# Performance work log

Measured on AMD Instinct MI355X. Metric: run time of the kernel, lower is better.

Reference implementation:

```python
import jax, jax.numpy as jnp
import numpy as np
from jax import lax

N, D, M, H = 8192, 32, 8, 128
ATOL = 1e-5
RTOL = 1e-5
MAX_STEPS = 10   # bounded adaptive dopri5 iterations (accept/reject with masking)
DT0 = 0.25


def setup_inputs() -> dict:
    key = jax.random.key(0)
    ks = jax.random.split(key, 6)
    p = lambda k, shape, s: jax.random.normal(k, shape, jnp.float32) * s
    return {
        "z": jax.random.normal(ks[0], (N, D), jnp.float32),
        "G_w": p(ks[1], (M, D), 0.3),
        "W1": p(ks[2], (H, D), (1.0 / D) ** 0.5),
        "b1": jnp.zeros((H,), jnp.float32),
        "W2": p(ks[3], (H, H), (1.0 / H) ** 0.5),
        "b2": jnp.zeros((H,), jnp.float32),
        "W3": p(ks[4], (D, H), (1.0 / H) ** 0.5),
        "b3": jnp.zeros((D,), jnp.float32),
        "T": jnp.ones((1,), jnp.float32),
    }


def qpnf_forward(z, G_w, W1, b1, W2, b2, W3, b3, T):
    d = z.shape[1]

    def mlp(x):  # dF network: d -> 128 -> 128 -> d
        h = jax.nn.relu(x @ W1.T + b1)
        h = jax.nn.relu(h @ W2.T + b2)
        return h @ W3.T + b3

    # G is linear (no bias) so jacrev(G)(x) == G_w for every sample; the batched
    # dG @ dG^T solves collapse to one shared (m,m) solve / (d,d) projector.
    A = G_w @ G_w.T                       # (m, m)
    AinvG = jnp.linalg.solve(A, G_w)      # (m, d) = A^{-1} W
    P = G_w.T @ AinvG                     # (d, d) null-space projector W^T A^{-1} W
    IP = jnp.eye(d, dtype=z.dtype) - P
    trP = jnp.trace(P)

    jac_mlp = jax.vmap(jax.jacrev(lambda xi: mlp(xi[None, :])[0]))  # (N,d,d)

    def f(y):  # augmented state y = [x | logp], dlogp/dt = -div(dx/dx)
        x = y[:, :d]
        dF = mlp(x)                        # (N, d)
        g = x @ G_w.T                      # (N, m)
        dz = -(dF @ IP) - g @ AinvG        # -(eta_J) - (eta_C)
        JdF = jac_mlp(x)                   # (N, d, d)
        # J_f = -(I-P) JdF - P  ->  dlogp = -trace(J_f)
        dlogp = jnp.einsum('jk,nkj->n', IP, JdF) + trP
        return jnp.concatenate([dz, dlogp[:, None]], axis=1)

    def rk_step(y, dt):  # Dormand-Prince 5(4)
        k1 = f(y)
        k2 = f(y + dt * (0.2 * k1))
        k3 = f(y + dt * (3/40 * k1 + 9/40 * k2))
        k4 = f(y + dt * (44/45 * k1 - 56/15 * k2 + 32/9 * k3))
        k5 = f(y + dt * (19372/6561 * k1 - 25360/2187 * k2 + 64448/6561 * k3 - 212/729 * k4))
        k6 = f(y + dt * (9017/3168 * k1 - 355/33 * k2 + 46732/5247 * k3 + 49/176 * k4 - 5103/18656 * k5))
        y1 = y + dt * (35/384 * k1 + 500/1113 * k3 + 125/192 * k4 - 2187/6784 * k5 + 11/84 * k6)
        k7 = f(y1)
        err = dt * ((35/384 - 5179/57600) * k1 + (500/1113 - 7571/16695) * k3
                    + (125/192 - 393/640) * k4 + (-2187/6784 + 92097/339200) * k5
                    + (11/84 - 187/2100) * k6 - (1/40) * k7)
        return y1, err

    t1 = 2.0 * T[0]  # eval path: integration_times[-1] *= 2
    y0 = jnp.concatenate([z, jnp.zeros((z.shape[0], 1), z.dtype)], axis=1)

    def body(carry, _):
        t, dt, y = carry
        done = t >= t1 - 1e-9
        dtc = jnp.where(done, jnp.asarray(1e-3, z.dtype), jnp.minimum(dt, t1 - t))
        y1, ev = rk_step(y, dtc)
        tol = ATOL + RTOL * jnp.maximum(jnp.abs(y), jnp.abs(y1))
        errn = jnp.sqrt(jnp.mean((ev / tol) ** 2))
        accept = jnp.logical_and(~done, errn <= 1.0)
        y_new = jnp.where(accept, y1, y)
        t_new = jnp.where(accept, t + dtc, t)
        factor = jnp.clip(0.9 * errn ** (-0.2), 0.2, 10.0)
        dt_new = jnp.where(done, dt, jnp.clip(dtc * factor, 1e-6, t1))
        dt_new = lax.stop_gradient(dt_new)
        return (t_new, dt_new, y_new), None

    init = (jnp.asarray(0.0, z.dtype), jnp.asarray(DT0, z.dtype), y0)
    (_, _, yT), _ = lax.scan(body, init, None, length=MAX_STEPS)
    return yT[:, :d]


def reference(z, G_w, W1, b1, W2, b2, W3, b3, T):
    return qpnf_forward(z, G_w, W1, b1, W2, b2, W3, b3, T)
```

## Files before the change

kernel.cpp:

```cpp
#include <hip/hip_runtime.h>
#include <hip/hip_cooperative_groups.h>
#include <math.h>

namespace cg = cooperative_groups;
typedef float4 f4;
typedef float2 f2;
typedef float v2f __attribute__((ext_vector_type(2)));

#define NT 512
#define RB 32

#define WS_WR    0
#define WS_PART  32768
#define WS_TOTAL 35328

#define L_W1T   0
#define L_C3T   4096
#define L_PT    8320
#define L_XW    9472
#define L_H1W   10496
#define L_H2W   14592
#define L_KZ    18688
#define L_KL    26752
#define L_YZ    26976
#define L_Y1Z   28128
#define L_YL    29280
#define L_Y1L   29312
#define L_B1    29344
#define L_B2    29472
#define L_C0    29600
#define L_GS    29632
#define L_AAUG  29888
#define L_AINVG 30016
#define L_MISC  30272
#define LDS_FLOATS 30276
#define L_RED   L_H1W
#define L_P     L_H2W
#define L_IP    (L_H2W + 1024)
#define L_IPW3  L_KZ

__device__ const float ACO[5][5] = {
  { 0.2f, 0.f, 0.f, 0.f, 0.f },
  { (float)(3.0/40.0), (float)(9.0/40.0), 0.f, 0.f, 0.f },
  { (float)(44.0/45.0), (float)(-56.0/15.0), (float)(32.0/9.0), 0.f, 0.f },
  { (float)(19372.0/6561.0), (float)(-25360.0/2187.0), (float)(64448.0/6561.0), (float)(-212.0/729.0), 0.f },
  { (float)(9017.0/3168.0), (float)(-355.0/33.0), (float)(46732.0/5247.0), (float)(49.0/176.0), (float)(-5103.0/18656.0) }
};

#define B1C ((float)(35.0/384.0))
#define B3C ((float)(500.0/1113.0))
#define B4C ((float)(125.0/192.0))
#define B5C ((float)(-2187.0/6784.0))
#define B6C ((float)(11.0/84.0))

#define E1C ((float)(35.0/384.0 - 5179.0/57600.0))
#define E3C ((float)(500.0/1113.0 - 7571.0/16695.0))
#define E4C ((float)(125.0/192.0 - 393.0/640.0))
#define E5C ((float)(-2187.0/6784.0 + 92097.0/339200.0))
#define E6C ((float)(11.0/84.0 - 187.0/2100.0))
#define E7C ((float)(-1.0/40.0))

__device__ __forceinline__ f4 ld4(const float* p){ return *(const f4*)p; }
__device__ __forceinline__ void st4(float* p, f4 v){ *(f4*)p = v; }

__device__ __forceinline__ void pk_lo(v2f& d, v2f s, v2f b){
  asm("v_pk_fma_f32 %0, %1, %2, %0 op_sel:[0,0,0] op_sel_hi:[0,1,1]"
      : "+v"(d) : "v"(s), "v"(b));
}
__device__ __forceinline__ void pk_hi(v2f& d, v2f s, v2f b){
  asm("v_pk_fma_f32 %0, %1, %2, %0 op_sel:[1,0,0] op_sel_hi:[1,1,1]"
      : "+v"(d) : "v"(s), "v"(b));
}
__device__ __forceinline__ v2f vlo(f4 v){ v2f r; r.x = v.x; r.y = v.y; return r; }
__device__ __forceinline__ v2f vhi(f4 v){ v2f r; r.x = v.z; r.y = v.w; return r; }

__device__ __forceinline__ void assemble_x(float* lds, int tid, float dtc,
                                           const float* co, int np)
{
  const int w = tid >> 6, lane = tid & 63;
  const int r = lane >> 4;
  const int c = (lane << 1) & 31;
  const int o = (4 * w + r) * 36 + c;
  f2 y = *(const f2*)&lds[L_YZ + o];
  float sx = 0.f, sy = 0.f;
  for (int p = 0; p < np; p++){
    f2 kv = *(const f2*)&lds[L_KZ + p * 1152 + o];
    sx += co[p] * kv.x; sy += co[p] * kv.y;
  }
  float* XWp = &lds[L_XW + w * 128];
  XWp[(c + 0) * 4 + r] = y.x + dtc * sx;
  XWp[(c + 1) * 4 + r] = y.y + dtc * sy;
}

__device__ void eval_f(float* lds, const float* __restrict__ ws, int tid,
                       float trP, int kout)
{
  const int w = tid >> 6, lane = tid & 63;
  const int cg = lane & 31, kh = lane >> 5;
  float* XWp = &lds[L_XW  + w * 128];
  float* H1p = &lds[L_H1W + w * 512];
  float* H2p = &lds[L_H2W + w * 512];

  const f4* WR4 = (const f4*)&ws[WS_WR];
  const int kb = kh * 64;
  const int grot = (w & 1) << 3;
  f4 wbA[4], rbA[4], wbB[4], rbB[4];
  {
    const int kA = kb + grot * 4;
    const int kB = kb + (grot + 1) * 4;
#pragma unroll
    for (int u = 0; u < 4; u++){
      wbA[u] = WR4[(kA + u) * 64 + cg];
      rbA[u] = WR4[(kA + u) * 64 + 32 + cg];
      wbB[u] = WR4[(kB + u) * 64 + cg];
      rbB[u] = WR4[(kB + u) * 64 + 32 + cg];
    }
  }

  v2f a12[4][2];
#pragma unroll
  for (int i = 0; i < 4; i++)
#pragma unroll
    for (int jp = 0; jp < 2; jp++){ a12[i][jp].x = 0.f; a12[i][jp].y = 0.f; }
#pragma unroll 4
  for (int t = 0; t < 16; t++){
    const int k = kh * 16 + t;
    f4 xv = ld4(&XWp[k * 4]);
    f4 wv = ld4(&lds[L_W1T + k * 128 + 4 * cg]);
    v2f x0 = vlo(xv), x1 = vhi(xv);
    v2f wA = vlo(wv), wB = vhi(wv);
    pk_lo(a12[0][0], wA, x0); pk_lo(a12[0][1], wA, x1);
    pk_hi(a12[1][0], wA, x0); pk_hi(a12[1][1], wA, x1);
    pk_lo(a12[2][0], wB, x0); pk_lo(a12[2][1], wB, x1);
    pk_hi(a12[3][0], wB, x0); pk_hi(a12[3][1], wB, x1);
  }
  float a1s[4][4];
#pragma unroll
  for (int i = 0; i < 4; i++){
    a1s[i][0] = a12[i][0].x; a1s[i][1] = a12[i][0].y;
    a1s[i][2] = a12[i][1].x; a1s[i][3] = a12[i][1].y;
  }
#pragma unroll
  for (int i = 0; i < 4; i++)
#pragma unroll
    for (int j = 0; j < 4; j++) a1s[i][j] += __shfl_xor(a1s[i][j], 32);
  if (kh == 0){
    f4 b1v = ld4(&lds[L_B1 + 4 * cg]);
    const float* b1p = (const float*)&b1v;
#pragma unroll
    for (int i = 0; i < 4; i++){
      f4 hv; float* hp = (float*)&hv;
#pragma unroll
      for (int j = 0; j < 4; j++){
        float pre = a1s[i][j] + b1p[i];
        hp[j] = fmaxf(pre, 0.f);
      }
      st4(&H1p[(4 * cg + i) * 4], hv);
    }
  }

  v2f ah2[4][2], at2[4][2];
#pragma unroll
  for (int i = 0; i < 4; i++)
#pragma unroll
    for (int jp = 0; jp < 2; jp++){
      ah2[i][jp].x = 0.f; ah2[i][jp].y = 0.f;
      at2[i][jp].x = 0.f; at2[i][jp].y = 0.f;
    }
#pragma unroll 1
  for (int gp = 0; gp < 8; gp++){
    {
      f4 wc[4], rc[4];
#pragma unroll
      for (int u = 0; u < 4; u++){ wc[u] = wbA[u]; rc[u] = rbA[u]; }
      if (gp < 7){
        const int kn = kb + (((2 * gp + 2) + grot) & 15) * 4;
#pragma unroll
        for (int u = 0; u < 4; u++){
          wbA[u] = WR4[(kn + u) * 64 + cg];
          rbA[u] = WR4[(kn + u) * 64 + 32 + cg];
        }
      }
      const int kc = kb + ((2 * gp + grot) & 15) * 4;
#pragma unroll
      for (int u = 0; u < 4; u++){
        f4 av = ld4(&H1p[(kc + u) * 4]);
        v2f a0 = vlo(av), a1 = vhi(av);
        v2f m0, m1;
        m0.x = (a0.x > 0.f) ? 1.f : 0.f; m0.y = (a0.y > 0.f) ? 1.f : 0.f;
        m1.x = (a1.x > 0.f) ? 1.f : 0.f; m1.y = (a1.y > 0.f) ? 1.f : 0.f;
        v2f wA = vlo(wc[u]), wB = vhi(wc[u]);
        v2f rA = vlo(rc[u]), rB = vhi(rc[u]);
        pk_lo(ah2[0][0], wA, a0); pk_lo(ah2[0][1], wA, a1);
        pk_hi(ah2[1][0], wA, a0); pk_hi(ah2[1][1], wA, a1);
        pk_lo(ah2[2][0], wB, a0); pk_lo(ah2[2][1], wB, a1);
        pk_hi(ah2[3][0], wB, a0); pk_hi(ah2[3][1], wB, a1);
        pk_lo(at2[0][0], rA, m0); pk_lo(at2[0][1], rA, m1);
        pk_hi(at2[1][0], rA, m0); pk_hi(at2[1][1], rA, m1);
        pk_lo(at2[2][0], rB, m0); pk_lo(at2[2][1], rB, m1);
        pk_hi(at2[3][0], rB, m0); pk_hi(at2[3][1], rB, m1);
      }
    }
    {
      f4 wc[4], rc[4];
#pragma unroll
      for (int u = 0; u < 4; u++){ wc[u] = wbB[u]; rc[u] = rbB[u]; }
      if (gp < 7){
        const int kn = kb + (((2 * gp + 3) + grot) & 15) * 4;
#pragma unroll
        for (int u = 0; u < 4; u++){
          wbB[u] = WR4[(kn + u) * 64 + cg];
          rbB[u] = WR4[(kn + u) * 64 + 32 + cg];
        }
      }
      const int kc = kb + (((2 * gp + 1) + grot) & 15) * 4;
#pragma unroll
      for (int u = 0; u < 4; u++){
        f4 av = ld4(&H1p[(kc + u) * 4]);
        v2f a0 = vlo(av), a1 = vhi(av);
        v2f m0, m1;
        m0.x = (a0.x > 0.f) ? 1.f : 0.f; m0.y = (a0.y > 0.f) ? 1.f : 0.f;
        m1.x = (a1.x > 0.f) ? 1.f : 0.f; m1.y = (a1.y > 0.f) ? 1.f : 0.f;
        v2f wA = vlo(wc[u]), wB = vhi(wc[u]);
        v2f rA = vlo(rc[u]), rB = vhi(rc[u]);
        pk_lo(ah2[0][0], wA, a0); pk_lo(ah2[0][1], wA, a1);
        pk_hi(ah2[1][0], wA, a0); pk_hi(ah2[1][1], wA, a1);
        pk_lo(ah2[2][0], wB, a0); pk_lo(ah2[2][1], wB, a1);
        pk_hi(ah2[3][0], wB, a0); pk_hi(ah2[3][1], wB, a1);
        pk_lo(at2[0][0], rA, m0); pk_lo(at2[0][1], rA, m1);
        pk_hi(at2[1][0], rA, m0); pk_hi(at2[1][1], rA, m1);
        pk_lo(at2[2][0], rB, m0); pk_lo(at2[2][1], rB, m1);
        pk_hi(at2[3][0], rB, m0); pk_hi(at2[3][1], rB, m1);
      }
    }
  }
  float ah[4][4], at[4][4];
#pragma unroll
  for (int i = 0; i < 4; i++){
    ah[i][0] = ah2[i][0].x; ah[i][1] = ah2[i][0].y;
    ah[i][2] = ah2[i][1].x; ah[i][3] = ah2[i][1].y;
    at[i][0] = at2[i][0].x; at[i][1] = at2[i][0].y;
    at[i][2] = at2[i][1].x; at[i][3] = at2[i][1].y;
  }
#pragma unroll
  for (int i = 0; i < 4; i++)
#pragma unroll
    for (int j = 0; j < 4; j++){
      ah[i][j] += __shfl_xor(ah[i][j], 32);
      at[i][j] += __shfl_xor(at[i][j], 32);
    }

  f4 b2v = ld4(&lds[L_B2 + 4 * cg]);
  const float* b2p = (const float*)&b2v;
  float h2v[4][4]; float dl[4] = {0.f, 0.f, 0.f, 0.f};
#pragma unroll
  for (int i = 0; i < 4; i++)
#pragma unroll
    for (int j = 0; j < 4; j++){
      float pre = ah[i][j] + b2p[i];
      float hv = fmaxf(pre, 0.f);
      h2v[i][j] = hv;
      if (pre > 0.f) dl[j] += at[i][j];
    }
#pragma unroll
  for (int mk = 1; mk < 32; mk <<= 1){
#pragma unroll
    for (int j = 0; j < 4; j++) dl[j] += __shfl_xor(dl[j], mk, 64);
  }
  if (kh == 0){
#pragma unroll
    for (int i = 0; i < 4; i++){
      f4 hv; float* hp = (float*)&hv;
#pragma unroll
      for (int j = 0; j < 4; j++) hp[j] = h2v[i][j];
      st4(&H2p[(4 * cg + i) * 4], hv);
    }
    if (cg == 0){
#pragma unroll
      for (int j = 0; j < 4; j++)
        lds[L_KL + kout * 32 + 4 * w + j] = dl[j] + trP;
    }
  }

  v2f a3e[2], a3o[2];
  a3e[0].x=0.f;a3e[0].y=0.f;a3e[1].x=0.f;a3e[1].y=0.f;
  a3o[0].x=0.f;a3o[0].y=0.f;a3o[1].x=0.f;a3o[1].y=0.f;
  const int bb = kh * 64;
#pragma unroll 4
  for (int t = 0; t < 16; t++){
    f4 cv = ld4(&lds[L_C3T + cg * 132 + bb + 4 * t]);
    v2f cA = vlo(cv), cB = vhi(cv);
    { f4 av = ld4(&H2p[(bb + 4 * t + 0) * 4]);
      pk_lo(a3e[0], cA, vlo(av)); pk_lo(a3e[1], cA, vhi(av)); }
    { f4 av = ld4(&H2p[(bb + 4 * t + 1) * 4]);
      pk_hi(a3o[0], cA, vlo(av)); pk_hi(a3o[1], cA, vhi(av)); }
    { f4 av = ld4(&H2p[(bb + 4 * t + 2) * 4]);
      pk_lo(a3e[0], cB, vlo(av)); pk_lo(a3e[1], cB, vhi(av)); }
    { f4 av = ld4(&H2p[(bb + 4 * t + 3) * 4]);
      pk_hi(a3o[0], cB, vlo(av)); pk_hi(a3o[1], cB, vhi(av)); }
  }
  const int qq = kh * 16;
#pragma unroll
  for (int t = 0; t < 4; t++){
    f4 pv = ld4(&lds[L_PT + cg * 36 + qq + 4 * t]);
    v2f pA = vlo(pv), pB = vhi(pv);
    { f4 av = ld4(&XWp[(qq + 4 * t + 0) * 4]);
      pk_lo(a3e[0], pA, vlo(av)); pk_lo(a3e[1], pA, vhi(av)); }
    { f4 av = ld4(&XWp[(qq + 4 * t + 1) * 4]);
      pk_hi(a3o[0], pA, vlo(av)); pk_hi(a3o[1], pA, vhi(av)); }
    { f4 av = ld4(&XWp[(qq + 4 * t + 2) * 4]);
      pk_lo(a3e[0], pB, vlo(av)); pk_lo(a3e[1], pB, vhi(av)); }
    { f4 av = ld4(&XWp[(qq + 4 * t + 3) * 4]);
      pk_hi(a3o[0], pB, vlo(av)); pk_hi(a3o[1], pB, vhi(av)); }
  }
  float a3[4];
  a3[0] = a3e[0].x + a3o[0].x; a3[1] = a3e[0].y + a3o[0].y;
  a3[2] = a3e[1].x + a3o[1].x; a3[3] = a3e[1].y + a3o[1].y;
#pragma unroll
  for (int j = 0; j < 4; j++) a3[j] += __shfl_xor(a3[j], 32);
  if (kh == 0){
    float c0v = lds[L_C0 + cg];
#pragma unroll
    for (int j = 0; j < 4; j++)
      lds[L_KZ + kout * 1152 + (4 * w + j) * 36 + cg] = -(a3[j] + c0v);
  }
}

__global__ void __launch_bounds__(NT, 2)
qpnf_kernel(const float* __restrict__ z, const float* __restrict__ Gw,
            const float* __restrict__ W1g, const float* __restrict__ b1g,
            const float* __restrict__ W2g, const float* __restrict__ b2g,
            const float* __restrict__ W3g, const float* __restrict__ b3g,
            const float* __restrict__ Tg, float* __restrict__ out,
            float* __restrict__ ws)
{
  __shared__ float lds[LDS_FLOATS];
  const int tid = threadIdx.x;
  const int bid = blockIdx.x;
  const int r0 = bid * RB;
  cg::grid_group grid = cg::this_grid();

  for (int i = 0; i < 8; i++){
    int idx = tid + i * NT;
    int h = idx >> 5, j = idx & 31;
    lds[L_W1T + j * 128 + h] = W1g[idx];
  }
  if (tid < 128){ lds[L_B1 + tid] = b1g[tid]; lds[L_B2 + tid] = b2g[tid]; }
  if (tid < 256) lds[L_GS + tid] = Gw[tid];
  __syncthreads();

  if (tid < 64){
    int i = tid >> 3, j = tid & 7;
    float s = 0.f;
    for (int k = 0; k < 32; k++) s += lds[L_GS + i * 32 + k] * lds[L_GS + j * 32 + k];
    lds[L_AAUG + i * 16 + j] = s;
    lds[L_AAUG + i * 16 + 8 + j] = (i == j) ? 1.f : 0.f;
  }
  __syncthreads();
  if (tid == 0){
    float* A = &lds[L_AAUG];
    for (int c = 0; c < 8; c++){
      int p = c; float mx = fabsf(A[c * 16 + c]);
      for (int r = c + 1; r < 8; r++){
        float v = fabsf(A[r * 16 + c]);
        if (v > mx){ mx = v; p = r; }
      }
      if (p != c)
        for (int q = 0; q < 16; q++){ float t = A[c*16+q]; A[c*16+q] = A[p*16+q]; A[p*16+q] = t; }
      float pv = 1.0f / A[c * 16 + c];
      for (int q = 0; q < 16; q++) A[c * 16 + q] *= pv;
      for (int r = 0; r < 8; r++) if (r != c){
        float fct = A[r * 16 + c];
        for (int q = 0; q < 16; q++) A[r * 16 + q] -= fct * A[c * 16 + q];
      }
    }
  }
  __syncthreads();
  if (tid < 256){
    int m = tid >> 5, d = tid & 31;
    float s = 0.f;
    for (int q = 0; q < 8; q++) s += lds[L_AAUG + m * 16 + 8 + q] * lds[L_GS + q * 32 + d];
    lds[L_AINVG + m * 32 + d] = s;
  }
  __syncthreads();
  for (int i4 = 0; i4 < 2; i4++){
    int idx = tid + i4 * NT;
    int i = idx >> 5, j = idx & 31;
    float s = 0.f;
    for (int m = 0; m < 8; m++) s += lds[L_GS + m * 32 + i] * lds[L_AINVG + m * 32 + j];
    lds[L_P + i * 32 + j] = s;
  }
  __syncthreads();
  float* IPl = &lds[L_IP];
  for (int i4 = 0; i4 < 2; i4++){
    int idx = tid + i4 * NT;
    int i = idx >> 5, j = idx & 31;
    IPl[i * 32 + j] = ((i == j) ? 1.f : 0.f) - lds[L_P + i * 32 + j];
  }
  if (tid == 0){
    float s = 0.f;
    for (int i = 0; i < 32; i++) s += lds[L_P + i * 32 + i];
    lds[L_MISC] = s;
  }
  __syncthreads();
  for (int i4 = 0; i4 < 8; i4++){
    int idx = tid + i4 * NT;
    int b = idx & 127, c = idx >> 7;
    float s = 0.f;
    for (int i = 0; i < 32; i++) s += W3g[i * 128 + b] * IPl[i * 32 + c];
    lds[L_C3T + c * 132 + b] = s;
  }
  for (int i4 = 0; i4 < 2; i4++){
    int idx = tid + i4 * NT;
    int c = idx >> 5, q = idx & 31;
    lds[L_PT + c * 36 + q] = lds[L_P + q * 32 + c];
  }
  if (tid < 32){
    float s = 0.f;
    for (int i = 0; i < 32; i++) s += b3g[i] * IPl[i * 32 + tid];
    lds[L_C0 + tid] = s;
  }
  for (int i4 = 0; i4 < 8; i4++){
    int idx = tid + i4 * NT;
    int j = idx >> 7, b = idx & 127;
    float s = 0.f;
    for (int k = 0; k < 32; k++) s += IPl[j * 32 + k] * W3g[k * 128 + b];
    lds[L_IPW3 + j * 128 + b] = s;
  }
  __syncthreads();
  if (bid < 128 && tid < 128){
    int a = bid;
    float s = 0.f;
    for (int j = 0; j < 32; j++) s += W1g[a * 32 + j] * lds[L_IPW3 + j * 128 + tid];
    ws[WS_WR + a * 256 + 128 + tid] = s * W2g[tid * 128 + a];
  }
  if (bid >= 128 && tid < 128){
    int a = bid - 128;
    ws[WS_WR + a * 256 + tid] = W2g[tid * 128 + a];
  }
  if (tid < 256){
    const int r = tid >> 3, jj = (tid & 7) * 4;
    st4(&lds[L_YZ + r * 36 + jj], ld4(&z[(r0 + r) * 32 + jj]));
  }
  if (tid < RB) lds[L_YL + tid] = 0.f;

  const float trP = lds[L_MISC];
  const float t1 = 2.0f * Tg[0];

  grid.sync();

  float t_cur = 0.f, dt_cur = 0.25f;
  bool prev_acc = false;

  for (int step = 0; step < 10; step++){
    if (t_cur >= t1 - 1e-9f) break;
    const float dtc = fminf(dt_cur, t1 - t_cur);

    for (int s = 1; s <= 6; s++){
      if (s == 1 && step > 0){
        if (prev_acc){
          const int w = tid >> 6, lane = tid & 63;
          const int r = lane >> 4, c = (lane << 1) & 31;
          const int o = (4 * w + r) * 36 + c;
          *(f2*)&lds[L_KZ + o] = *(const f2*)&lds[L_KZ + 6 * 1152 + o];
          if (lane < 4) lds[L_KL + 4 * w + lane] = lds[L_KL + 6 * 32 + 4 * w + lane];
        }
        continue;
      }
      assemble_x(lds, tid, dtc, ACO[s >= 2 ? s - 2 : 0], s - 1);
      eval_f(lds, ws, tid, trP, s - 1);
    }

    __syncthreads();
    if (tid < 256){
      const int r = tid >> 3, jj = (tid & 7) * 4;
      const int o = r * 36 + jj;
      f4 y   = ld4(&lds[L_YZ + o]);
      f4 k1v = ld4(&lds[L_KZ + 0 * 1152 + o]);
      f4 k3v = ld4(&lds[L_KZ + 2 * 1152 + o]);
      f4 k4v = ld4(&lds[L_KZ + 3 * 1152 + o]);
      f4 k5v = ld4(&lds[L_KZ + 4 * 1152 + o]);
      f4 k6v = ld4(&lds[L_KZ + 5 * 1152 + o]);
      f4 x;
      x.x = y.x + dtc * (B1C*k1v.x + B3C*k3v.x + B4C*k4v.x + B5C*k5v.x + B6C*k6v.x);
      x.y = y.y + dtc * (B1C*k1v.y + B3C*k3v.y + B4C*k4v.y + B5C*k5v.y + B6C*k6v.y);
      x.z = y.z + dtc * (B1C*k1v.z + B3C*k3v.z + B4C*k4v.z + B5C*k5v.z + B6C*k6v.z);
      x.w = y.w + dtc * (B1C*k1v.w + B3C*k3v.w + B4C*k4v.w + B5C*k5v.w + B6C*k6v.w);
      st4(&lds[L_Y1Z + o], x);
      float* XWp = &lds[L_XW + (r >> 2) * 128];
      const int rr = r & 3;
      XWp[(jj + 0) * 4 + rr] = x.x;
      XWp[(jj + 1) * 4 + rr] = x.y;
      XWp[(jj + 2) * 4 + rr] = x.z;
      XWp[(jj + 3) * 4 + rr] = x.w;
    }
    if (tid < RB){
      float s = B1C * lds[L_KL + 0*32 + tid] + B3C * lds[L_KL + 2*32 + tid]
              + B4C * lds[L_KL + 3*32 + tid] + B5C * lds[L_KL + 4*32 + tid]
              + B6C * lds[L_KL + 5*32 + tid];
      lds[L_Y1L + tid] = lds[L_YL + tid] + dtc * s;
    }
    __syncthreads();
    eval_f(lds, ws, tid, trP, 6);
    __syncthreads();

    float sacc = 0.f;
    if (tid < 256){
      const int r = tid >> 3, jj = (tid & 7) * 4;
      const int o = r * 36 + jj;
      f4 k1v = ld4(&lds[L_KZ + 0 * 1152 + o]);
      f4 k3v = ld4(&lds[L_KZ + 2 * 1152 + o]);
      f4 k4v = ld4(&lds[L_KZ + 3 * 1152 + o]);
      f4 k5v = ld4(&lds[L_KZ + 4 * 1152 + o]);
      f4 k6v = ld4(&lds[L_KZ + 5 * 1152 + o]);
      f4 k7v = ld4(&lds[L_KZ + 6 * 1152 + o]);
      f4 yv  = ld4(&lds[L_YZ + o]);
      f4 y1v = ld4(&lds[L_Y1Z + o]);
      float ev, tol, q;
      ev = dtc * (E1C*k1v.x + E3C*k3v.x + E4C*k4v.x + E5C*k5v.x + E6C*k6v.x + E7C*k7v.x);
      tol = 1e-5f + 1e-5f * fmaxf(fabsf(yv.x), fabsf(y1v.x)); q = ev / tol; sacc += q * q;
      ev = dtc * (E1C*k1v.y + E3C*k3v.y + E4C*k4v.y + E5C*k5v.y + E6C*k6v.y + E7C*k7v.y);
      tol = 1e-5f + 1e-5f * fmaxf(fabsf(yv.y), fabsf(y1v.y)); q = ev / tol; sacc += q * q;
      ev = dtc * (E1C*k1v.z + E3C*k3v.z + E4C*k4v.z + E5C*k5v.z + E6C*k6v.z + E7C*k7v.z);
      tol = 1e-5f + 1e-5f * fmaxf(fabsf(yv.z), fabsf(y1v.z)); q = ev / tol; sacc += q * q;
      ev = dtc * (E1C*k1v.w + E3C*k3v.w + E4C*k4v.w + E5C*k5v.w + E6C*k6v.w + E7C*k7v.w);
      tol = 1e-5f + 1e-5f * fmaxf(fabsf(yv.w), fabsf(y1v.w)); q = ev / tol; sacc += q * q;
    }
    if (tid < RB){
      float evl = dtc * (E1C * lds[L_KL + 0*32 + tid] + E3C * lds[L_KL + 2*32 + tid]
                + E4C * lds[L_KL + 3*32 + tid] + E5C * lds[L_KL + 4*32 + tid]
                + E6C * lds[L_KL + 5*32 + tid] + E7C * lds[L_KL + 6*32 + tid]);
      float toll = 1e-5f + 1e-5f * fmaxf(fabsf(lds[L_YL + tid]), fabsf(lds[L_Y1L + tid]));
      float ql = evl / toll; sacc += ql * ql;
    }
#pragma unroll
    for (int mk = 1; mk < 64; mk <<= 1) sacc += __shfl_xor(sacc, mk, 64);
    if ((tid & 63) == 0) lds[L_RED + (tid >> 6)] = sacc;
    __syncthreads();
    if (tid == 0){
      float s = lds[L_RED+0] + lds[L_RED+1] + lds[L_RED+2] + lds[L_RED+3]
              + lds[L_RED+4] + lds[L_RED+5] + lds[L_RED+6] + lds[L_RED+7];
      ws[WS_PART + step * 256 + bid] = s;
    }

    grid.sync();

    float ps = 0.f;
    if (tid < 256) ps = ws[WS_PART + step * 256 + tid];
#pragma unroll
    for (int mk = 1; mk < 64; mk <<= 1) ps += __shfl_xor(ps, mk, 64);
    if (tid < 256 && (tid & 63) == 0) lds[L_RED + (tid >> 6)] = ps;
    __syncthreads();
    const float errn = sqrtf((lds[L_RED+0] + lds[L_RED+1] + lds[L_RED+2] + lds[L_RED+3])
                             / 270336.0f);
    __syncthreads();

    const bool accept = (errn <= 1.0f);
    if (accept){
      const int w = tid >> 6, lane = tid & 63;
      const int r = lane >> 4, c = (lane << 1) & 31;
      const int o = (4 * w + r) * 36 + c;
      *(f2*)&lds[L_YZ + o] = *(const f2*)&lds[L_Y1Z + o];
      if (lane < 4) lds[L_YL + 4 * w + lane] = lds[L_Y1L + 4 * w + lane];
      t_cur += dtc;
    }
    float fac = 0.9f * powf(errn, -0.2f);
    fac = fminf(fmaxf(fac, 0.2f), 10.0f);
    dt_cur = fminf(fmaxf(dtc * fac, 1e-6f), t1);
    prev_acc = accept;
  }

  __syncthreads();
  if (tid < 256){
    const int r = tid >> 3, jj = (tid & 7) * 4;
    st4(&out[(r0 + r) * 32 + jj], ld4(&lds[L_YZ + r * 36 + jj]));
  }
}

extern "C" void kernel_launch(void* const* d_in, const int* in_sizes, int n_in,
                              void* d_out, int out_size, void* d_ws, size_t ws_size,
                              hipStream_t stream)
{
  (void)in_sizes; (void)n_in; (void)out_size;
  const float* z  = (const float*)d_in[0];
  const float* Gw = (const float*)d_in[1];
  const float* W1 = (const float*)d_in[2];
  const float* b1 = (const float*)d_in[3];
  const float* W2 = (const float*)d_in[4];
  const float* b2 = (const float*)d_in[5];
  const float* W3 = (const float*)d_in[6];
  const float* b3 = (const float*)d_in[7];
  const float* T  = (const float*)d_in[8];
  float* out = (float*)d_out;
  float* ws  = (float*)d_ws;
  if (ws_size < (size_t)WS_TOTAL * sizeof(float)) return;

  void* args[] = { (void*)&z, (void*)&Gw, (void*)&W1, (void*)&b1, (void*)&W2,
                   (void*)&b2, (void*)&W3, (void*)&b3, (void*)&T, (void*)&out,
                   (void*)&ws };
  hipLaunchCooperativeKernel((const void*)qpnf_kernel, dim3(256), dim3(NT),
                             args, 0, stream);
}
```

Measured before the change: 1.330 ms.

## Stage W2/R weight tiles through double-buffered LDS instead of per-wave global loads

Layer-2 weights and the Jacobian-propagation weights were previously fetched from global memory by every wave, each holding its own register prefetch buffers. Now the block loads each 8-row chunk once cooperatively, stores it into a double-buffered LDS region, and all waves read it from LDS, with a __syncthreads per chunk. This cuts redundant global/L2 traffic and register pressure from the prefetch buffers. In exchange it adds 32KB of LDS, which may lower occupancy, and adds block-wide barriers inside the hot loop.

After: 1.278 ms. 4.0% less time.

```diff
diff --git a/kernel.cpp b/kernel.cpp
--- a/kernel.cpp
+++ b/kernel.cpp
@@ -33,7 +33,8 @@
 #define L_AAUG  29888
 #define L_AINVG 30016
 #define L_MISC  30272
-#define LDS_FLOATS 30276
+#define L_WRS   30276
+#define LDS_FLOATS (30276 + 8192)
 #define L_RED   L_H1W
 #define L_P     L_H2W
 #define L_IP    (L_H2W + 1024)
@@ -97,24 +98,19 @@
 {
   const int w = tid >> 6, lane = tid & 63;
   const int cg = lane & 31, kh = lane >> 5;
-  float* XWp = &lds[L_XW  + w * 128];
+  float* XWp = &lds[L_XW  + w * 512 / 4];
   float* H1p = &lds[L_H1W + w * 512];
   float* H2p = &lds[L_H2W + w * 512];
 
   const f4* WR4 = (const f4*)&ws[WS_WR];
-  const int kb = kh * 64;
-  const int grot = (w & 1) << 3;
-  f4 wbA[4], rbA[4], wbB[4], rbB[4];
+  const int sp = tid >> 8;
+  const int st = (tid >> 5) & 7;
+  const int sc = tid & 31;
+  f4 sa, sb;
   {
-    const int kA = kb + grot * 4;
-    const int kB = kb + (grot + 1) * 4;
-#pragma unroll
-    for (int u = 0; u < 4; u++){
-      wbA[u] = WR4[(kA + u) * 64 + cg];
-      rbA[u] = WR4[(kA + u) * 64 + 32 + cg];
-      wbB[u] = WR4[(kB + u) * 64 + cg];
-      rbB[u] = WR4[(kB + u) * 64 + 32 + cg];
-    }
+    const int krow = sp * 64 + st;
+    sa = WR4[krow * 64 + sc];
+    sb = WR4[krow * 64 + 32 + sc];
   }
 
   v2f a12[4][2];
@@ -158,6 +154,11 @@
       st4(&H1p[(4 * cg + i) * 4], hv);
     }
   }
+  {
+    float* d = &lds[L_WRS + sp * 2048 + st * 256 + 4 * sc];
+    st4(d, sa); st4(d + 128, sb);
+  }
+  __syncthreads();
 
   v2f ah2[4][2], at2[4][2];
 #pragma unroll
@@ -168,71 +169,38 @@
       at2[i][jp].x = 0.f; at2[i][jp].y = 0.f;
     }
 #pragma unroll 1
-  for (int gp = 0; gp < 8; gp++){
-    {
-      f4 wc[4], rc[4];
-#pragma unroll
-      for (int u = 0; u < 4; u++){ wc[u] = wbA[u]; rc[u] = rbA[u]; }
-      if (gp < 7){
-        const int kn = kb + (((2 * gp + 2) + grot) & 15) * 4;
-#pragma unroll
-        for (int u = 0; u < 4; u++){
-          wbA[u] = WR4[(kn + u) * 64 + cg];
-          rbA[u] = WR4[(kn + u) * 64 + 32 + cg];
-        }
-      }
-      const int kc = kb + ((2 * gp + grot) & 15) * 4;
-#pragma unroll
-      for (int u = 0; u < 4; u++){
-        f4 av = ld4(&H1p[(kc + u) * 4]);
-        v2f a0 = vlo(av), a1 = vhi(av);
-        v2f m0, m1;
-        m0.x = (a0.x > 0.f) ? 1.f : 0.f; m0.y = (a0.y > 0.f) ? 1.f : 0.f;
-        m1.x = (a1.x > 0.f) ? 1.f : 0.f; m1.y = (a1.y > 0.f) ? 1.f : 0.f;
-        v2f wA = vlo(wc[u]), wB = vhi(wc[u]);
-        v2f rA = vlo(rc[u]), rB = vhi(rc[u]);
-        pk_lo(ah2[0][0], wA, a0); pk_lo(ah2[0][1], wA, a1);
-        pk_hi(ah2[1][0], wA, a0); pk_hi(ah2[1][1], wA, a1);
-        pk_lo(ah2[2][0], wB, a0); pk_lo(ah2[2][1], wB, a1);
-        pk_hi(ah2[3][0], wB, a0); pk_hi(ah2[3][1], wB, a1);
-        pk_lo(at2[0][0], rA, m0); pk_lo(at2[0][1], rA, m1);
-        pk_hi(at2[1][0], rA, m0); pk_hi(at2[1][1], rA, m1);
-        pk_lo(at2[2][0], rB, m0); pk_lo(at2[2][1], rB, m1);
-        pk_hi(at2[3][0], rB, m0); pk_hi(at2[3][1], rB, m1);
-      }
-    }
-    {
-      f4 wc[4], rc[4];
-#pragma unroll
-      for (int u = 0; u < 4; u++){ wc[u] = wbB[u]; rc[u] = rbB[u]; }
-      if (gp < 7){
-        const int kn = kb + (((2 * gp + 3) + grot) & 15) * 4;
-#pragma unroll
-        for (int u = 0; u < 4; u++){
-          wbB[u] = WR4[(kn + u) * 64 + cg];
-          rbB[u] = WR4[(kn + u) * 64 + 32 + cg];
-        }
-      }
-      const int kc = kb + (((2 * gp + 1) + grot) & 15) * 4;
-#pragma unroll
-      for (int u = 0; u < 4; u++){
-        f4 av = ld4(&H1p[(kc + u) * 4]);
-        v2f a0 = vlo(av), a1 = vhi(av);
-        v2f m0, m1;
-        m0.x = (a0.x > 0.f) ? 1.f : 0.f; m0.y = (a0.y > 0.f) ? 1.f : 0.f;
-        m1.x = (a1.x > 0.f) ? 1.f : 0.f; m1.y = (a1.y > 0.f) ? 1.f : 0.f;
-        v2f wA = vlo(wc[u]), wB = vhi(wc[u]);
-        v2f rA = vlo(rc[u]), rB = vhi(rc[u]);
-        pk_lo(ah2[0][0], wA, a0); pk_lo(ah2[0][1], wA, a1);
-        pk_hi(ah2[1][0], wA, a0); pk_hi(ah2[1][1], wA, a1);
-        pk_lo(ah2[2][0], wB, a0); pk_lo(ah2[2][1], wB, a1);
-        pk_hi(ah2[3][0], wB, a0); pk_hi(ah2[3][1], wB, a1);
-        pk_lo(at2[0][0], rA, m0); pk_lo(at2[0][1], rA, m1);
-        pk_hi(at2[1][0], rA, m0); pk_hi(at2[1][1], rA, m1);
-        pk_lo(at2[2][0], rB, m0); pk_lo(at2[2][1], rB, m1);
-        pk_hi(at2[3][0], rB, m0); pk_hi(at2[3][1], rB, m1);
-      }
-    }
+  for (int c = 0; c < 8; c++){
+    if (c < 7){
+      const int krow = sp * 64 + (c + 1) * 8 + st;
+      sa = WR4[krow * 64 + sc];
+      sb = WR4[krow * 64 + 32 + sc];
+    }
+    const float* WB = &lds[L_WRS + (c & 1) * 4096 + kh * 2048];
+#pragma unroll
+    for (int t = 0; t < 8; t++){
+      f4 wcv = ld4(&WB[t * 256 + 4 * cg]);
+      f4 rcv = ld4(&WB[t * 256 + 128 + 4 * cg]);
+      f4 av  = ld4(&H1p[(kh * 64 + c * 8 + t) * 4]);
+      v2f a0 = vlo(av), a1 = vhi(av);
+      v2f m0, m1;
+      m0.x = (a0.x > 0.f) ? 1.f : 0.f; m0.y = (a0.y > 0.f) ? 1.f : 0.f;
+      m1.x = (a1.x > 0.f) ? 1.f : 0.f; m1.y = (a1.y > 0.f) ? 1.f : 0.f;
+      v2f wA = vlo(wcv), wB2 = vhi(wcv);
+      v2f rA = vlo(rcv), rB = vhi(rcv);
+      pk_lo(ah2[0][0], wA, a0);  pk_lo(ah2[0][1], wA, a1);
+      pk_hi(ah2[1][0], wA, a0);  pk_hi(ah2[1][1], wA, a1);
+      pk_lo(ah2[2][0], wB2, a0); pk_lo(ah2[2][1], wB2, a1);
+      pk_hi(ah2[3][0], wB2, a0); pk_hi(ah2[3][1], wB2, a1);
+      pk_lo(at2[0][0], rA, m0);  pk_lo(at2[0][1], rA, m1);
+      pk_hi(at2[1][0], rA, m0);  pk_hi(at2[1][1], rA, m1);
+      pk_lo(at2[2][0], rB, m0);  pk_lo(at2[2][1], rB, m1);
+      pk_hi(at2[3][0], rB, m0);  pk_hi(at2[3][1], rB, m1);
+    }
+    if (c < 7){
+      float* d = &lds[L_WRS + ((c + 1) & 1) * 4096 + sp * 2048 + st * 256 + 4 * sc];
+      st4(d, sa); st4(d + 128, sb);
+    }
+    __syncthreads();
   }
   float ah[4][4], at[4][4];
 #pragma unroll
```
